# Kernel tuning notes

Measured on AMD Instinct MI355X. Metric: run time of the kernel, lower is better.

Reference implementation:

```python
import jax, jax.numpy as jnp
import numpy as np

E, H = 256, 4
DH = E // H                      # head dim 64
DHALF, N, R, K = 256, 16, 16, 5  # mamba d_inner//2, d_state, dt_rank, d_conv
B, L = 2, 2048


def _ln(x, g, b):
    m = jnp.mean(x, -1, keepdims=True)
    v = jnp.var(x, -1, keepdims=True)
    return (x - m) * jax.lax.rsqrt(v + 1e-5) * g + b


def _rotate_half(x):
    y = x.reshape(x.shape[:-1] + (-1, 2))
    return jnp.stack((-y[..., 1], y[..., 0]), -1).reshape(x.shape)


def _dwconv(x, w):  # x: (B,C,L), w: (C,1,K), depthwise 'same' conv, no bias (conv_bias//2 == 0)
    return jax.lax.conv_general_dilated(
        x, w, (1,), 'SAME', feature_group_count=x.shape[1],
        dimension_numbers=('NCH', 'OIH', 'NCH'))


def _selective_scan(x, dt, A_log, Bm, Cm, Dp, dt_bias):
    # x, dt: (B,Dh,L); Bm, Cm: (B,N,L); A_log: (Dh,N); Dp, dt_bias: (Dh,)
    A = -jnp.exp(A_log)
    delta = jax.nn.softplus(dt + dt_bias[None, :, None])
    seq = (jnp.moveaxis(delta, 2, 0), jnp.moveaxis(x, 2, 0),
           jnp.moveaxis(Bm, 2, 0), jnp.moveaxis(Cm, 2, 0))
    h0 = jnp.zeros((x.shape[0], A.shape[0], A.shape[1]), x.dtype)

    def step(h, inp):
        d_l, x_l, B_l, C_l = inp
        h = jnp.exp(d_l[:, :, None] * A) * h + (d_l * x_l)[:, :, None] * B_l[:, None, :]
        return h, jnp.einsum('bdn,bn->bd', h, C_l)

    _, ys = jax.lax.scan(step, h0, seq)
    return jnp.moveaxis(ys, 0, 2) + Dp[None, :, None] * x


def _forward(desc0, desc1, pe0, pe1, qkv_w, qkv_b, attn_out_w, attn_out_b,
             ma_ffn_w1, ma_ffn_b1, ma_ffn_g, ma_ffn_beta, ma_ffn_w2, ma_ffn_b2,
             m_in_w, m_convx_w, m_convz_w, m_xproj_w, m_dt_w, m_dt_b, m_Alog, m_D, m_out_w,
             ca_qk_w, ca_qk_b, ca_v_w, ca_v_b, ca_out_w, ca_out_b,
             ca_ffn_w1, ca_ffn_b1, ca_ffn_g, ca_ffn_beta, ca_ffn_w2, ca_ffn_b2):

    def mamba_twopath(x_in):
        xz = jnp.swapaxes(x_in @ m_in_w.T, 1, 2)           # (B, 2*Dh, L)
        xc, zc = xz[:, :DHALF], xz[:, DHALF:]
        xc = jax.nn.silu(_dwconv(xc, m_convx_w))
        zc = jax.nn.silu(_dwconv(zc, m_convz_w))
        x_dbl = jnp.einsum('bdl,kd->bkl', xc, m_xproj_w)   # (B, R+2N, L)
        # dt_proj applies its bias here AND the same bias is re-added inside the scan
        # (delta_bias), exactly as in the torch source.
        dt = jnp.einsum('brl,dr->bdl', x_dbl[:, :R], m_dt_w) + m_dt_b[None, :, None]
        Bm, Cm = x_dbl[:, R:R + N], x_dbl[:, R + N:]
        y = _selective_scan(xc, dt, m_Alog, Bm, Cm, m_D, m_dt_b)  # (B, Dh, L)
        return jnp.swapaxes(y, 1, 2) @ m_out_w.T, jnp.swapaxes(zc, 1, 2) @ m_out_w.T

    def ma_ffn(h):
        h = _ln(h @ ma_ffn_w1.T + ma_ffn_b1, ma_ffn_g, ma_ffn_beta)
        return jax.nn.gelu(h, approximate=False) @ ma_ffn_w2.T + ma_ffn_b2

    def mamba_attention(x, pe):
        b, l, _ = x.shape
        qkv = (x @ qkv_w.T + qkv_b).reshape(b, l, H, DH, 3)
        qkv = jnp.swapaxes(qkv, 1, 2)                       # (B,H,L,DH,3)
        q, k, v = qkv[..., 0], qkv[..., 1], qkv[..., 2]
        q = q * pe[0] + _rotate_half(q) * pe[1]
        k = k * pe[0] + _rotate_half(k) * pe[1]
        attn = jax.nn.softmax(jnp.einsum('bhid,bhjd->bhij', q, k) * DH ** -0.5, -1)
        o = jnp.einsum('bhij,bhjd->bhid', attn, v)
        o = jnp.swapaxes(o, 1, 2).reshape(b, l, E) @ attn_out_w.T + attn_out_b
        s_x, c_x = mamba_twopath(x)
        return x + ma_ffn(jnp.concatenate([x, o, s_x, c_x], -1))

    def ca_ffn(h):
        h = _ln(h @ ca_ffn_w1.T + ca_ffn_b1, ca_ffn_g, ca_ffn_beta)
        return jax.nn.gelu(h, approximate=False) @ ca_ffn_w2.T + ca_ffn_b2

    def split_heads(t):
        b, l, _ = t.shape
        return jnp.swapaxes(t.reshape(b, l, H, DH), 1, 2)

    def cross_attn(x0, x1):
        s = DH ** -0.25  # scale**0.5 applied to both qk0 and qk1
        qk0 = split_heads(x0 @ ca_qk_w.T + ca_qk_b) * s
        qk1 = split_heads(x1 @ ca_qk_w.T + ca_qk_b) * s
        v0 = split_heads(x0 @ ca_v_w.T + ca_v_b)
        v1 = split_heads(x1 @ ca_v_w.T + ca_v_b)
        sim = jnp.einsum('bhid,bhjd->bhij', qk0, qk1)       # (B,H,L0,L1)
        m0 = jnp.einsum('bhij,bhjd->bhid', jax.nn.softmax(sim, -1), v1)
        m1 = jnp.einsum('bhji,bhjd->bhid', jax.nn.softmax(sim, -2), v0)
        b, l = x0.shape[0], x0.shape[1]
        m0 = jnp.swapaxes(m0, 1, 2).reshape(b, l, E) @ ca_out_w.T + ca_out_b
        m1 = jnp.swapaxes(m1, 1, 2).reshape(b, x1.shape[1], E) @ ca_out_w.T + ca_out_b
        x0 = x0 + ca_ffn(jnp.concatenate([x0, m0], -1))
        x1 = x1 + ca_ffn(jnp.concatenate([x1, m1], -1))
        return x0, x1

    d0 = mamba_attention(desc0, pe0)
    d1 = mamba_attention(desc1, pe1)
    return cross_attn(d0, d1)


def setup_inputs():
    key = jax.random.key(0)
    ks = jax.random.split(key, 32)
    rn = lambda i, shape, s=0.02: jax.random.normal(ks[i], shape, jnp.float32) * s
    rng = np.random.default_rng(0)
    dt = np.exp(rng.uniform(size=DHALF) * (np.log(0.1) - np.log(0.001)) + np.log(0.001))
    inv_dt = dt + np.log(-np.expm1(-dt))
    return {
        'desc0': jax.random.normal(ks[0], (B, L, E), jnp.float32),
        'desc1': jax.random.normal(ks[1], (B, L, E), jnp.float32),
        'pe0': jax.random.normal(ks[2], (2, B, 1, L, DH), jnp.float32),
        'pe1': jax.random.normal(ks[3], (2, B, 1, L, DH), jnp.float32),
        'qkv_w': rn(4, (3 * E, E)), 'qkv_b': rn(5, (3 * E,)),
        'attn_out_w': rn(6, (E, E)), 'attn_out_b': rn(7, (E,)),
        'ma_ffn_w1': rn(8, (2 * E, 4 * E)), 'ma_ffn_b1': rn(9, (2 * E,)),
        'ma_ffn_g': jnp.ones((2 * E,), jnp.float32), 'ma_ffn_beta': jnp.zeros((2 * E,), jnp.float32),
        'ma_ffn_w2': rn(10, (E, 2 * E)), 'ma_ffn_b2': rn(11, (E,)),
        'm_in_w': rn(12, (2 * DHALF, E)),
        'm_convx_w': rn(13, (DHALF, 1, K), 0.2), 'm_convz_w': rn(14, (DHALF, 1, K), 0.2),
        'm_xproj_w': rn(15, (R + 2 * N, DHALF)),
        'm_dt_w': rn(16, (DHALF, R), R ** -0.5),
        'm_dt_b': jnp.asarray(inv_dt, jnp.float32),
        'm_Alog': jnp.log(jnp.broadcast_to(jnp.arange(1, N + 1, dtype=jnp.float32), (DHALF, N))),
        'm_D': jnp.ones((DHALF,), jnp.float32),
        'm_out_w': rn(17, (E, DHALF)),
        'ca_qk_w': rn(18, (E, E)), 'ca_qk_b': rn(19, (E,)),
        'ca_v_w': rn(20, (E, E)), 'ca_v_b': rn(21, (E,)),
        'ca_out_w': rn(22, (E, E)), 'ca_out_b': rn(23, (E,)),
        'ca_ffn_w1': rn(24, (2 * E, 2 * E)), 'ca_ffn_b1': rn(25, (2 * E,)),
        'ca_ffn_g': jnp.ones((2 * E,), jnp.float32), 'ca_ffn_beta': jnp.zeros((2 * E,), jnp.float32),
        'ca_ffn_w2': rn(26, (E, 2 * E)), 'ca_ffn_b2': rn(27, (E,)),
    }


def reference(desc0, desc1, pe0, pe1, qkv_w, qkv_b, attn_out_w, attn_out_b,
              ma_ffn_w1, ma_ffn_b1, ma_ffn_g, ma_ffn_beta, ma_ffn_w2, ma_ffn_b2,
              m_in_w, m_convx_w, m_convz_w, m_xproj_w, m_dt_w, m_dt_b, m_Alog, m_D, m_out_w,
              ca_qk_w, ca_qk_b, ca_v_w, ca_v_b, ca_out_w, ca_out_b,
              ca_ffn_w1, ca_ffn_b1, ca_ffn_g, ca_ffn_beta, ca_ffn_w2, ca_ffn_b2):
    return _forward(desc0, desc1, pe0, pe1, qkv_w, qkv_b, attn_out_w, attn_out_b,
                    ma_ffn_w1, ma_ffn_b1, ma_ffn_g, ma_ffn_beta, ma_ffn_w2, ma_ffn_b2,
                    m_in_w, m_convx_w, m_convz_w, m_xproj_w, m_dt_w, m_dt_b, m_Alog, m_D, m_out_w,
                    ca_qk_w, ca_qk_b, ca_v_w, ca_v_b, ca_out_w, ca_out_b,
                    ca_ffn_w1, ca_ffn_b1, ca_ffn_g, ca_ffn_beta, ca_ffn_w2, ca_ffn_b2)
```

## Files before the change

kernel.cpp:

```cpp
#include <hip/hip_runtime.h>

typedef unsigned short u16;
typedef short s16;
typedef s16 s16x8 __attribute__((ext_vector_type(8)));
typedef float f32x4 __attribute__((ext_vector_type(4)));

__device__ __forceinline__ float bf2f(u16 u){
  union { unsigned int i; float f; } v; v.i = ((unsigned int)u) << 16; return v.f;
}
__device__ __forceinline__ u16 f2bf(float f){
  union { float f; unsigned int u; } v; v.f = f;
  unsigned int r = (v.u + 0x7fffu + ((v.u >> 16) & 1u)) >> 16;
  return (u16)r;
}
__device__ __forceinline__ unsigned int cvtpk(float lo, float hi){
  unsigned int d;
  asm("v_cvt_pk_bf16_f32 %0, %1, %2" : "=v"(d) : "v"(lo), "v"(hi));
  return d;
}
__device__ __forceinline__ uint4 pack8(float4 a0, float4 a1){
  uint4 v;
  v.x = cvtpk(a0.x, a0.y); v.y = cvtpk(a0.z, a0.w);
  v.z = cvtpk(a1.x, a1.y); v.w = cvtpk(a1.z, a1.w);
  return v;
}
__device__ __forceinline__ float gelu_f(float x){
  return 0.5f * x * (1.f + erff(x * 0.70710678118654752440f));
}
__device__ __forceinline__ float ldw(const void* p, long i, int fl){
  return fl ? bf2f(((const u16*)p)[i]) : ((const float*)p)[i];
}
__device__ __forceinline__ float4 ldw4(const void* p, long i, int fl){
  if (fl){
    ushort4 w = *(const ushort4*)((const u16*)p + i);
    return make_float4(bf2f(w.x), bf2f(w.y), bf2f(w.z), bf2f(w.w));
  }
  return *(const float4*)((const float*)p + i);
}

template<int C>
__device__ __forceinline__ float dppf(float x){
  return __int_as_float(__builtin_amdgcn_update_dpp(0, __float_as_int(x), C, 0xf, 0xf, true));
}
__device__ __forceinline__ float dppmax16(float v){
  v = fmaxf(v, dppf<0xB1>(v));
  v = fmaxf(v, dppf<0x4E>(v));
  v = fmaxf(v, dppf<0x141>(v));
  v = fmaxf(v, dppf<0x140>(v));
  return v;
}
__device__ __forceinline__ float dppsum16(float v){
  v += dppf<0xB1>(v);
  v += dppf<0x4E>(v);
  v += dppf<0x141>(v);
  v += dppf<0x140>(v);
  return v;
}

__global__ __launch_bounds__(256) void k_sniff(const unsigned int* __restrict__ w,
                                               int n, int* __restrict__ flag){
  __shared__ int cnt[256];
  int c = 0;
  for (int i = threadIdx.x; i < n; i += 256){
    unsigned e = (w[i] >> 7) & 0xFFu;
    c += (e >= 120u && e <= 127u) ? 1 : 0;
  }
  cnt[threadIdx.x] = c; __syncthreads();
  for (int s = 128; s > 0; s >>= 1){
    if (threadIdx.x < s) cnt[threadIdx.x] += cnt[threadIdx.x + s];
    __syncthreads();
  }
  if (threadIdx.x == 0) flag[0] = (2 * cnt[0] > n) ? 1 : 0;
  if (threadIdx.x == 1) flag[1] = 0;
}

__global__ __launch_bounds__(256) void k_pad(
  const void* __restrict__ wx, const void* __restrict__ wd,
  const void* __restrict__ bd,
  float* __restrict__ px, float* __restrict__ pd, float* __restrict__ pb,
  const int* __restrict__ flagp)
{
  int fl = *flagp;
  int i = blockIdx.x * 256 + threadIdx.x;
  if (i < 16384){
    int r = i >> 8, c = i & 255;
    px[i] = (r < 48) ? ldw(wx, r*256 + c, fl) : 0.f;
  } else if (i < 32768){
    int j = i - 16384;
    int n = j >> 6, k = j & 63;
    pd[j] = (k < 16) ? ldw(wd, n*16 + k, fl) : 0.f;
  } else if (i < 33024){
    pb[i - 32768] = ldw(bd, i - 32768, fl);
  }
}

__global__ __launch_bounds__(256) void k_gemm_mfma(
  const void* __restrict__ A, int aflidx, int lda, int K, int N,
  const void* __restrict__ W, const void* __restrict__ W2, int nsplit, int wflidx,
  const void* __restrict__ bias,
  float* __restrict__ Cf, u16* __restrict__ Cb, int ldc,
  float* __restrict__ C2, int ldc2,
  const void* __restrict__ resid, int rflidx, int ldr,
  const void* __restrict__ csrc, int cflidx, float* __restrict__ cdst,
  float oscale, int act_gelu, int outmode, const int* __restrict__ flagp)
{
  const int fl  = flagp[0];
  const int afl = flagp[aflidx];
  const int wfl = flagp[wflidx];
  const int rfl = flagp[rflidx];
  const int cfl = flagp[cflidx];
  __shared__ u16 As[64*72];
  __shared__ u16 Bs[64*72];
  const int tid = threadIdx.x;
  const int w = tid >> 6, lane = tid & 63, quad = lane >> 4, m = lane & 15;
  const int m0 = blockIdx.y << 6, n0 = blockIdx.x << 6;
  const int srow = tid >> 2, sc0 = (tid & 3) << 4;
  const int reg2 = (n0 >= nsplit);
  const void* Wp = reg2 ? W2 : W;
  const int nbase = reg2 ? nsplit : 0;

  f32x4 acc[4];
  #pragma unroll
  for (int ct = 0; ct < 4; ++ct) acc[ct] = (f32x4){0.f,0.f,0.f,0.f};

  for (int k0 = 0; k0 < K; k0 += 64){
    {
      long ab = (long)(m0 + srow) * lda + k0 + sc0;
      if (afl && !act_gelu){
        #pragma unroll
        for (int g = 0; g < 2; ++g)
          *(uint4*)&As[srow*72 + sc0 + g*8] = *(const uint4*)((const u16*)A + ab + g*8);
      } else {
        #pragma unroll
        for (int g = 0; g < 2; ++g){
          float4 a0 = ldw4(A, ab + g*8, afl);
          float4 a1 = ldw4(A, ab + g*8 + 4, afl);
          if (act_gelu){
            a0.x=gelu_f(a0.x); a0.y=gelu_f(a0.y); a0.z=gelu_f(a0.z); a0.w=gelu_f(a0.w);
            a1.x=gelu_f(a1.x); a1.y=gelu_f(a1.y); a1.z=gelu_f(a1.z); a1.w=gelu_f(a1.w);
          }
          *(uint4*)&As[srow*72 + sc0 + g*8] = pack8(a0, a1);
        }
      }
    }
    {
      long wb = (long)(n0 + srow - nbase) * K + k0 + sc0;
      if (wfl){
        #pragma unroll
        for (int g = 0; g < 2; ++g)
          *(uint4*)&Bs[srow*72 + sc0 + g*8] = *(const uint4*)((const u16*)Wp + wb + g*8);
      } else {
        #pragma unroll
        for (int g = 0; g < 2; ++g){
          float4 b0 = *(const float4*)((const float*)Wp + wb + g*8);
          float4 b1 = *(const float4*)((const float*)Wp + wb + g*8 + 4);
          *(uint4*)&Bs[srow*72 + sc0 + g*8] = pack8(b0, b1);
        }
      }
    }
    __syncthreads();

    s16x8 av[2];
    #pragma unroll
    for (int s = 0; s < 2; ++s)
      av[s] = *(const s16x8*)&As[(w*16 + m)*72 + s*32 + quad*8];
    #pragma unroll
    for (int ct = 0; ct < 4; ++ct)
      #pragma unroll
      for (int s = 0; s < 2; ++s){
        s16x8 bv = *(const s16x8*)&Bs[(ct*16 + m)*72 + s*32 + quad*8];
        acc[ct] = __builtin_amdgcn_mfma_f32_16x16x32_bf16(av[s], bv, acc[ct], 0, 0, 0);
      }
    __syncthreads();
  }

  #pragma unroll
  for (int r = 0; r < 4; ++r){
    int gm = m0 + w*16 + quad*4 + r;
    #pragma unroll
    for (int ct = 0; ct < 4; ++ct){
      int gn = n0 + ct*16 + m;
      float v = acc[ct][r];
      if (reg2){
        C2[(long)gm * ldc2 + (gn - nsplit)] = v;
      } else if (outmode == 4){
        float bv = ldw(bias, gn, wfl);
        float dl = v + bv + bv;
        float delta = (dl > 20.f) ? dl : __logf(1.f + __expf(dl));
        Cf[(long)gm * ldc + gn] = delta;
        C2[(long)gm * ldc2 + gn] = delta * ldw(resid, (long)gm * ldr + gn, rfl);
      } else {
        if (bias) v += ldw(bias, gn, wfl);
        v *= oscale;
        if (resid) v += ldw(resid, (long)gm * ldr + gn, rfl);
        long off = (long)gm * ldc + gn;
        if (outmode == 2){
          if (fl) Cb[off] = f2bf(v); else Cf[off] = v;
        } else if (outmode == 3){
          Cb[off] = f2bf(v);
        } else {
          Cf[off] = v;
        }
        if (cdst) cdst[(long)gm * ldc + gn] = ldw(csrc, (long)gm * 256 + gn, cfl);
      }
    }
  }
}

struct GB8 {
  const float* A[8]; const void* W[8]; const void* bias[8];
  float* Cf[8]; u16* Cb[8]; const void* resid[8];
  const void* csrc[8]; float* cdst[8]; float osc[8];
  int cfl[8]; int wkoff[8]; int rfli[8];
};

__global__ __launch_bounds__(256) void k_gemmb(
  GB8 gb, int lda, int K, int N, int ldc, int ldr, int ldwq,
  int act_gelu, int outmode, const int* __restrict__ flagp)
{
  const int fl = flagp[0];
  const int z = blockIdx.z;
  const float* A = gb.A[z]; const void* W = gb.W[z]; const void* bias = gb.bias[z];
  float* Cf = gb.Cf[z]; u16* Cb = gb.Cb[z]; const void* resid = gb.resid[z];
  const void* csrc = gb.csrc[z]; float* cdst = gb.cdst[z];
  const float osc = gb.osc[z];
  const int cfl = flagp[gb.cfl[z]];
  const int rfl = flagp[gb.rfli[z]];
  const int wkoff = gb.wkoff[z];

  __shared__ u16 As[64*72];
  __shared__ u16 Bs[64*72];
  const int tid = threadIdx.x;
  const int w = tid >> 6, lane = tid & 63, quad = lane >> 4, m = lane & 15;
  const int m0 = blockIdx.y << 6, n0 = blockIdx.x << 6;
  const int srow = tid >> 2, sc0 = (tid & 3) << 4;

  f32x4 acc[4];
  #pragma unroll
  for (int ct = 0; ct < 4; ++ct) acc[ct] = (f32x4){0.f,0.f,0.f,0.f};

  for (int k0 = 0; k0 < K; k0 += 64){
    {
      const float* ar = A + (long)(m0 + srow) * lda + k0 + sc0;
      #pragma unroll
      for (int g = 0; g < 2; ++g){
        float4 a0 = *(const float4*)(ar + g*8);
        float4 a1 = *(const float4*)(ar + g*8 + 4);
        if (act_gelu){
          a0.x=gelu_f(a0.x); a0.y=gelu_f(a0.y); a0.z=gelu_f(a0.z); a0.w=gelu_f(a0.w);
          a1.x=gelu_f(a1.x); a1.y=gelu_f(a1.y); a1.z=gelu_f(a1.z); a1.w=gelu_f(a1.w);
        }
        *(uint4*)&As[srow*72 + sc0 + g*8] = pack8(a0, a1);
      }
    }
    {
      long wb = (long)(n0 + srow) * ldwq + wkoff + k0 + sc0;
      if (fl){
        #pragma unroll
        for (int g = 0; g < 2; ++g)
          *(uint4*)&Bs[srow*72 + sc0 + g*8] = *(const uint4*)((const u16*)W + wb + g*8);
      } else {
        #pragma unroll
        for (int g = 0; g < 2; ++g){
          float4 b0 = *(const float4*)((const float*)W + wb + g*8);
          float4 b1 = *(const float4*)((const float*)W + wb + g*8 + 4);
          *(uint4*)&Bs[srow*72 + sc0 + g*8] = pack8(b0, b1);
        }
      }
    }
    __syncthreads();

    s16x8 av[2];
    #pragma unroll
    for (int s = 0; s < 2; ++s)
      av[s] = *(const s16x8*)&As[(w*16 + m)*72 + s*32 + quad*8];
    #pragma unroll
    for (int ct = 0; ct < 4; ++ct)
      #pragma unroll
      for (int s = 0; s < 2; ++s){
        s16x8 bv = *(const s16x8*)&Bs[(ct*16 + m)*72 + s*32 + quad*8];
        acc[ct] = __builtin_amdgcn_mfma_f32_16x16x32_bf16(av[s], bv, acc[ct], 0, 0, 0);
      }
    __syncthreads();
  }

  #pragma unroll
  for (int r = 0; r < 4; ++r){
    int gm = m0 + w*16 + quad*4 + r;
    #pragma unroll
    for (int ct = 0; ct < 4; ++ct){
      int gn = n0 + ct*16 + m;
      float v = acc[ct][r];
      if (bias) v += ldw(bias, gn, fl);
      v *= osc;
      if (resid) v += ldw(resid, (long)gm * ldr + gn, rfl);
      long off = (long)gm * ldc + gn;
      if (outmode == 2){
        if (fl) Cb[off] = f2bf(v); else Cf[off] = v;
      } else if (outmode == 3){
        Cb[off] = f2bf(v);
      } else {
        Cf[off] = v;
      }
      if (cdst) cdst[(long)gm * ldc + gn] = ldw(csrc, (long)gm * 256 + gn, cfl);
    }
  }
}

__global__ __launch_bounds__(256) void k_rope(
  const float* __restrict__ qkv0, const float* __restrict__ qkv1,
  const void* __restrict__ pe0, const void* __restrict__ pe1,
  u16* __restrict__ q, u16* __restrict__ k, u16* __restrict__ v,
  int L, int B, int H, const int* __restrict__ flagp)
{
  int fl = *flagp;
  int tid = threadIdx.x;
  int lq = tid >> 6, d = tid & 63;
  int l = blockIdx.x * 4 + lq;
  int bh = blockIdx.y;
  int dsc = bh >> 3;
  int bh7 = bh & 7;
  int b = bh7 >> 2, h = bh7 & 3;
  const float* qkv = dsc ? qkv1 : qkv0;
  const void* pe = dsc ? pe1 : pe0;
  const float* row = qkv + ((long)b * L + l) * 768 + h * 192;
  float qv = row[d*3+0], kv = row[d*3+1], vv = row[d*3+2];
  int dn = (d & 1) ? (d - 1) : (d + 1);
  float qn = row[dn*3+0], kn = row[dn*3+1];
  float rq = (d & 1) ? qn : -qn;
  float rk = (d & 1) ? kn : -kn;
  long peo = ((long)b * L + l) * 64 + d;
  float p0 = ldw(pe, peo, fl);
  float p1 = ldw(pe, (long)B * L * 64 + peo, fl);
  long o = ((long)bh * L + l) * 64 + d;
  q[o] = f2bf((qv * p0 + rq * p1) * 0.125f);
  k[o] = f2bf(kv * p0 + rk * p1);
  v[o] = f2bf(vv);
}

__global__ __launch_bounds__(256, 8) void k_attn_mfma(
  const u16* __restrict__ Q, long qsb, long qsh, long qsl,
  const u16* __restrict__ Kp, long ksb, long ksh, long ksl,
  const u16* __restrict__ Vp, long vsb, long vsh, long vsl,
  float* __restrict__ Opart, float* __restrict__ mpart, float* __restrict__ lpart,
  int L, int H, int kchunk)
{
  __shared__ u16 Kt[64*72];
  __shared__ u16 Vt[64*72];
  __shared__ u16 Ps[64*72];
  const int tid  = threadIdx.x;
  const int w    = tid >> 6;
  const int lane = tid & 63;
  const int quad = lane >> 4;
  const int m    = lane & 15;
  const int bh = blockIdx.y, b = bh / H, h = bh % H;
  const int iq0 = blockIdx.x * 64;
  const int z = blockIdx.z;
  const long BHL = (long)gridDim.y * L;

  const u16* Qb = Q  + b*qsb + h*qsh;
  const u16* Kb = Kp + b*ksb + h*ksh;
  const u16* Vb = Vp + b*vsb + h*vsh;

  s16x8 aq[2];
  {
    const u16* qr = Qb + (long)(iq0 + w*16 + m) * qsl + quad*8;
    aq[0] = *(const s16x8*)(qr);
    aq[1] = *(const s16x8*)(qr + 32);
  }

  f32x4 o_acc[4];
  #pragma unroll
  for (int nt = 0; nt < 4; ++nt) o_acc[nt] = (f32x4){0.f,0.f,0.f,0.f};
  float mrow[4] = {-1e30f,-1e30f,-1e30f,-1e30f};
  float lrow[4] = {0.f,0.f,0.f,0.f};

  const int srow = tid >> 2, sc0 = (tid & 3) << 4;
  const int kg = tid & 15;
  const int dg = tid >> 4;
  const int vcb = ((((dg >> 2) * 2) + (kg >> 1)) & 7) * 8 + (kg & 1) * 4;
  const int modd = m & 1;
  const int pcolb = m & 6;
  const int jend = z * kchunk + kchunk;

  for (int j0 = z * kchunk; j0 < jend; j0 += 64){
    {
      const u16* kr = Kb + (long)(j0 + srow) * ksl + sc0;
      *(uint4*)&Kt[srow*72 + sc0]     = *(const uint4*)kr;
      *(uint4*)&Kt[srow*72 + sc0 + 8] = *(const uint4*)(kr + 8);
      const u16* vr = Vb + (long)(j0 + 4*kg) * vsl + 4*dg;
      ushort4 r0 = *(const ushort4*)(vr);
      ushort4 r1 = *(const ushort4*)(vr + vsl);
      ushort4 r2 = *(const ushort4*)(vr + 2*vsl);
      ushort4 r3 = *(const ushort4*)(vr + 3*vsl);
      u16* vt = &Vt[(4*dg)*72 + vcb];
      *(ushort4*)(vt)       = make_ushort4(r0.x, r1.x, r2.x, r3.x);
      *(ushort4*)(vt + 72)  = make_ushort4(r0.y, r1.y, r2.y, r3.y);
      *(ushort4*)(vt + 144) = make_ushort4(r0.z, r1.z, r2.z, r3.z);
      *(ushort4*)(vt + 216) = make_ushort4(r0.w, r1.w, r2.w, r3.w);
    }
    __syncthreads();

    float sv[4][4];
    #pragma unroll
    for (int ct = 0; ct < 4; ++ct){
      f32x4 acc = (f32x4){0.f,0.f,0.f,0.f};
      #pragma unroll
      for (int s = 0; s < 2; ++s){
        s16x8 bk = *(const s16x8*)&Kt[(ct*16 + m)*72 + s*32 + quad*8];
        acc = __builtin_amdgcn_mfma_f32_16x16x32_bf16(aq[s], bk, acc, 0, 0, 0);
      }
      #pragma unroll
      for (int r = 0; r < 4; ++r) sv[ct][r] = acc[r];
    }

    float v0s[4];
    int need = 0;
    #pragma unroll
    for (int r = 0; r < 4; ++r){
      float v0 = fmaxf(fmaxf(sv[0][r], sv[1][r]), fmaxf(sv[2][r], sv[3][r]));
      v0 = dppmax16(v0);
      v0s[r] = v0;
      need |= (v0 > mrow[r] + 8.f) ? 1 : 0;
    }
    if (__any(need)){
      float alpha[4];
      #pragma unroll
      for (int r = 0; r < 4; ++r){
        float mn = fmaxf(mrow[r], v0s[r]);
        alpha[r] = __expf(mrow[r] - mn);
        mrow[r] = mn;
        lrow[r] *= alpha[r];
      }
      #pragma unroll
      for (int nt = 0; nt < 4; ++nt)
        #pragma unroll
        for (int r = 0; r < 4; ++r) o_acc[nt][r] *= alpha[r];
    }
    float rsum[4] = {0.f,0.f,0.f,0.f};
    #pragma unroll
    for (int ct = 0; ct < 4; ++ct)
      #pragma unroll
      for (int r = 0; r < 4; ++r){
        float p = __expf(sv[ct][r] - mrow[r]);
        sv[ct][r] = p;
        rsum[r] += p;
      }
    #pragma unroll
    for (int r = 0; r < 4; ++r)
      lrow[r] += dppsum16(rsum[r]);

    #pragma unroll
    for (int ct = 0; ct < 4; ++ct){
      const int kb = (2*w + 2*ct + (m >> 3)) & 7;
      const int col = (kb << 3) | pcolb;
      #pragma unroll
      for (int rr = 0; rr < 2; ++rr){
        float nb_lo = dppf<0xB1>(sv[ct][rr]);
        float nb_hi = dppf<0xB1>(sv[ct][2+rr]);
        float lo = modd ? nb_hi       : sv[ct][rr];
        float hi = modd ? sv[ct][2+rr] : nb_lo;
        unsigned int pk = cvtpk(lo, hi);
        int row = w*16 + quad*4 + rr + 2*modd;
        *(unsigned int*)&Ps[row*72 + col] = pk;
      }
    }
    asm volatile("s_waitcnt lgkmcnt(0)" ::: "memory");

    s16x8 ap[2];
    #pragma unroll
    for (int s = 0; s < 2; ++s)
      ap[s] = *(const s16x8*)&Ps[(w*16 + m)*72 + (((2*w + 4*s + quad) & 7) << 3)];
    #pragma unroll
    for (int nt = 0; nt < 4; ++nt)
      #pragma unroll
      for (int s = 0; s < 2; ++s){
        s16x8 bv = *(const s16x8*)&Vt[(nt*16 + m)*72 + (((2*nt + 4*s + quad) & 7) << 3)];
        o_acc[nt] = __builtin_amdgcn_mfma_f32_16x16x32_bf16(ap[s], bv, o_acc[nt], 0, 0, 0);
      }
    __syncthreads();
  }

  const long zOoff = (long)z * BHL * 64;
  #pragma unroll
  for (int r = 0; r < 4; ++r){
    int iq = iq0 + w*16 + quad*4 + r;
    long rowid = ((long)b*L + iq) * H + h;
    #pragma unroll
    for (int nt = 0; nt < 4; ++nt)
      Opart[zOoff + rowid*64 + nt*16 + m] = o_acc[nt][r];
    if (m == 0){
      mpart[(long)z*BHL + rowid] = mrow[r];
      lpart[(long)z*BHL + rowid] = lrow[r];
    }
  }
}

__global__ __launch_bounds__(256) void k_attn_comb(
  const float* Opart, const float* mpart, const float* lpart,
  float* O, long BHL)
{
  long i = (long)blockIdx.x * 256 + threadIdx.x;
  long row = i >> 6;
  float mv[4];
  float M = -1e30f;
  #pragma unroll
  for (int z = 0; z < 4; ++z){
    mv[z] = mpart[(long)z*BHL + row];
    M = fmaxf(M, mv[z]);
  }
  long N64 = BHL * 64;
  float T = 0.f, acc = 0.f;
  #pragma unroll
  for (int z = 0; z < 4; ++z){
    float wz = __expf(mv[z] - M);
    T   += lpart[(long)z*BHL + row] * wz;
    acc += Opart[(long)z*N64 + i] * wz;
  }
  O[i] = acc / T;
}

__global__ __launch_bounds__(256) void k_conv2(
  const float* __restrict__ xz,
  const void* __restrict__ wx, const void* __restrict__ wz,
  float* __restrict__ outx, float* __restrict__ outz,
  int L, const int* __restrict__ flagp)
{
  int fl = *flagp;
  int c = threadIdx.x;
  int bl = blockIdx.x; int b = bl / L, l = bl % L;
  int choff = blockIdx.y ? 256 : 0;
  const void* w = blockIdx.y ? wz : wx;
  float* out = blockIdx.y ? outz : outx;
  const float* base = xz + ((long)b * L) * 512 + choff + c;
  float s = 0.f;
  #pragma unroll
  for (int kk = 0; kk < 5; ++kk){
    int ll = l + kk - 2;
    if (ll >= 0 && ll < L) s += base[(long)ll * 512] * ldw(w, c*5 + kk, fl);
  }
  out[((long)b * L + l) * 256 + c] = s / (1.f + __expf(-s));
}

#define SC_CS 64
#define SC_NC 32

__global__ __launch_bounds__(256) void k_scan1(
  const float* __restrict__ delta, const float* __restrict__ dxc,
  const float* __restrict__ xdbl, const void* __restrict__ Alog,
  float* __restrict__ E_out, float* __restrict__ F_out,
  int L, const int* __restrict__ flagp)
{
  int fl = *flagp;
  int tid = threadIdx.x;
  int g = tid >> 4, n = tid & 15;
  int gid = blockIdx.x * 16 + g;
  int chunk = gid & (SC_NC - 1);
  int p = gid >> 5;
  int b = p >> 8, d = p & 255;
  float A = -__expf(ldw(Alog, d*16 + n, fl));
  const float* dtp = delta + (long)b*L*256 + d;
  const float* dxp = dxc   + (long)b*L*256 + d;
  const float* xdb = xdbl + (long)b*L*64;
  int l0 = chunk * SC_CS;
  float E = 1.f, F = 0.f;
  for (int i = 0; i < SC_CS; i += 4){
    float e[4], u[4];
    #pragma unroll
    for (int j = 0; j < 4; ++j){
      int l = l0 + i + j;
      e[j] = __expf(dtp[(long)l*256] * A);
      u[j] = dxp[(long)l*256] * xdb[l*64 + 16 + n];
    }
    F = e[0]*F + u[0]; F = e[1]*F + u[1];
    F = e[2]*F + u[2]; F = e[3]*F + u[3];
    E *= (e[0]*e[1]) * (e[2]*e[3]);
  }
  long idx = (long)(p*16 + n) * SC_NC + chunk;
  E_out[idx] = E; F_out[idx] = F;
}

__global__ __launch_bounds__(256) void k_scan2(
  const float* __restrict__ E, const float* __restrict__ F,
  float* __restrict__ Hin)
{
  int pn = blockIdx.x * 256 + threadIdx.x;
  const float* Ep = E + (long)pn * SC_NC;
  const float* Fp = F + (long)pn * SC_NC;
  float* Hp = Hin + (long)pn * SC_NC;
  float h = 0.f;
  #pragma unroll
  for (int c = 0; c < SC_NC; ++c){
    Hp[c] = h;
    h = Ep[c] * h + Fp[c];
  }
}

__global__ __launch_bounds__(256) void k_scan3(
  const float* __restrict__ delta, const float* __restrict__ dxc,
  const float* __restrict__ xc, const float* __restrict__ xdbl,
  const void* __restrict__ Alog, const void* __restrict__ Dp,
  const float* __restrict__ Hin, float* __restrict__ y,
  int L, const int* __restrict__ flagp)
{
  int fl = *flagp;
  int tid = threadIdx.x;
  int g = tid >> 4, n = tid & 15;
  int gid = blockIdx.x * 16 + g;
  int chunk = gid & (SC_NC - 1);
  int p = gid >> 5;
  int b = p >> 8, d = p & 255;
  float A = -__expf(ldw(Alog, d*16 + n, fl));
  float Dv = ldw(Dp, d, fl);
  const float* dtp = delta + (long)b*L*256 + d;
  const float* dxp = dxc   + (long)b*L*256 + d;
  const float* xcb = xc    + (long)b*L*256 + d;
  const float* xdb = xdbl + (long)b*L*64;
  float* yb = y + (long)b*L*256 + d;
  long idx = (long)(p*16 + n) * SC_NC + chunk;
  float h = Hin[idx];
  int l0 = chunk * SC_CS;
  for (int i = 0; i < SC_CS; i += 4){
    float e[4], u[4], cm[4], xv[4];
    #pragma unroll
    for (int j = 0; j < 4; ++j){
      int l = l0 + i + j;
      e[j]  = __expf(dtp[(long)l*256] * A);
      u[j]  = dxp[(long)l*256] * xdb[l*64 + 16 + n];
      cm[j] = xdb[l*64 + 32 + n];
      xv[j] = xcb[(long)l*256];
    }
    float s0, s1, s2, s3;
    h = e[0]*h + u[0]; s0 = h * cm[0];
    h = e[1]*h + u[1]; s1 = h * cm[1];
    h = e[2]*h + u[2]; s2 = h * cm[2];
    h = e[3]*h + u[3]; s3 = h * cm[3];
    s0 += __shfl_xor(s0, 1, 16); s1 += __shfl_xor(s1, 1, 16);
    s2 += __shfl_xor(s2, 1, 16); s3 += __shfl_xor(s3, 1, 16);
    s0 += __shfl_xor(s0, 2, 16); s1 += __shfl_xor(s1, 2, 16);
    s2 += __shfl_xor(s2, 2, 16); s3 += __shfl_xor(s3, 2, 16);
    s0 += __shfl_xor(s0, 4, 16); s1 += __shfl_xor(s1, 4, 16);
    s2 += __shfl_xor(s2, 4, 16); s3 += __shfl_xor(s3, 4, 16);
    s0 += __shfl_xor(s0, 8, 16); s1 += __shfl_xor(s1, 8, 16);
    s2 += __shfl_xor(s2, 8, 16); s3 += __shfl_xor(s3, 8, 16);
    if (n < 4){
      float out = (n == 0) ? s0 + Dv*xv[0] : (n == 1) ? s1 + Dv*xv[1]
                : (n == 2) ? s2 + Dv*xv[2] : s3 + Dv*xv[3];
      yb[(long)(l0 + i + n)*256] = out;
    }
  }
}

__global__ __launch_bounds__(256) void k_ln2(
  float* __restrict__ hA, const float* __restrict__ hA2,
  float* __restrict__ hB, const float* __restrict__ hB2,
  const void* __restrict__ g, const void* __restrict__ beta,
  const int* __restrict__ flagp)
{
  int fl = *flagp;
  int r = blockIdx.x * 4 + (threadIdx.x >> 6);
  float* hbase = (r < 4096) ? hA : hB;
  const float* h2base = (r < 4096) ? hA2 : hB2;
  int row = r & 4095;
  int lane = threadIdx.x & 63;
  float* hr = hbase + (long)row * 512;
  const float* h2r = h2base + (long)row * 512;
  float v[8]; float s = 0.f, ss = 0.f;
  #pragma unroll
  for (int i = 0; i < 8; ++i){
    v[i] = hr[lane + 64*i] + h2r[lane + 64*i];
    s += v[i]; ss += v[i]*v[i];
  }
  #pragma unroll
  for (int off = 1; off < 64; off <<= 1){ s += __shfl_xor(s, off); ss += __shfl_xor(ss, off); }
  float mean = s * (1.f/512.f);
  float var  = ss * (1.f/512.f) - mean * mean;
  float rs = rsqrtf(var + 1e-5f);
  #pragma unroll
  for (int i = 0; i < 8; ++i){
    int c = lane + 64*i;
    hr[c] = (v[i] - mean) * rs * ldw(g, c, fl) + ldw(beta, c, fl);
  }
}

extern "C" void kernel_launch(void* const* d_in, const int* in_sizes, int n_in,
                              void* d_out, int out_size, void* d_ws, size_t ws_size,
                              hipStream_t stream)
{
  const int B_ = 2, L_ = 2048, H_ = 4;
  const long BLE = (long)B_ * L_ * 256;
  const long BHLb = 2L * B_ * H_ * L_;
  const long BHLc = (long)B_ * H_ * L_;

  int* flagp = (int*)d_ws;
  float* base = (float*)d_ws + 64;

  float* cat0   = base + 0*BLE;
  float* cat1   = base + 3*BLE;
  float* xz01   = base + 6*BLE;
  u16*   q01    = (u16*)(base + 10*BLE);
  u16*   k01    = (u16*)(base + 11*BLE);
  u16*   v01    = (u16*)(base + 12*BLE);
  float* Opart  = base + 13*BLE;
  float* ob01   = base + 21*BLE;
  float* mml    = base + 23*BLE;
  float* mll    = mml + 4*32768;
  float* xc01   = base + 24*BLE;
  float* zc01   = base + 26*BLE;
  float* xdbl01 = base + 28*BLE;
  float* delta01= base + 29*BLE;
  float* dxc01  = base + 31*BLE;
  float* scE    = base + 33*BLE;
  float* scF    = scE + 524288;
  float* scH    = scF + 524288;
  float* y01    = base + 35*BLE;
  float* catc0  = base + 37*BLE;
  float* catc1  = base + 41*BLE;
  float* h0     = base + 45*BLE;
  float* part0  = base + 47*BLE;
  float* h1     = base + 49*BLE;
  float* part1  = base + 51*BLE;
  float* dbuf0  = base + 53*BLE;
  float* dbuf1  = base + 54*BLE;
  u16*   qc     = (u16*)(base + 55*BLE);
  u16*   kc     = qc + 1048576;
  u16*   vc     = kc + 1048576;
  u16*   oc     = vc + 1048576;
  float* catA   = base + 57*BLE;
  float* catB   = base + 59*BLE;
  float* px     = base + 61*BLE;
  float* pd     = px + 16384;
  float* pb     = pd + 16384;

  const void* in[35];
  for (int i = 0; i < 35 && i < n_in; ++i) in[i] = d_in[i];

  k_sniff<<<1, 256, 0, stream>>>((const unsigned int*)in[0], 2048, flagp);
  k_pad<<<130, 256, 0, stream>>>(in[17], in[18], in[19], px, pd, pb, flagp);

  const int BIG = 1 << 30;
  const long sbP = (long)H_ * L_ * 64, shP = (long)L_ * 64, slP = 64;
  const long sbF = (long)L_ * 256,     shF = 64,            slF = 256;
  const int kchunk = L_ / 4;

  k_gemm_mfma<<<dim3(20, 64), 256, 0, stream>>>(
      in[0], 0, 256, 256, 1280, in[4], in[14], 768, 0, in[5],
      cat0, nullptr, 768, xz01, 512,
      nullptr, 1, 0, nullptr, 1, nullptr, 1.f, 0, 0, flagp);
  k_gemm_mfma<<<dim3(20, 64), 256, 0, stream>>>(
      in[1], 0, 256, 256, 1280, in[4], in[14], 768, 0, in[5],
      cat1, nullptr, 768, xz01 + 2*BLE, 512,
      nullptr, 1, 0, nullptr, 1, nullptr, 1.f, 0, 0, flagp);
  k_rope<<<dim3(L_/4, 16), 256, 0, stream>>>(cat0, cat1, in[2], in[3],
      q01, k01, v01, L_, B_, H_, flagp);
  k_attn_mfma<<<dim3(L_/64, 16, 4), 256, 0, stream>>>(
      q01, sbP, shP, slP, k01, sbP, shP, slP, v01, sbP, shP, slP,
      Opart, mml, mll, L_, H_, kchunk);
  k_attn_comb<<<8192, 256, 0, stream>>>(Opart, mml, mll, ob01, BHLb);
  k_conv2<<<dim3(2*B_*L_, 2), 256, 0, stream>>>(xz01, in[15], in[16], xc01, zc01, L_, flagp);
  k_gemm_mfma<<<dim3(1, 128), 256, 0, stream>>>(
      xc01, 1, 256, 256, 64, px, nullptr, BIG, 1, nullptr,
      xdbl01, nullptr, 64, nullptr, 0,
      nullptr, 1, 0, nullptr, 1, nullptr, 1.f, 0, 0, flagp);
  k_gemm_mfma<<<dim3(4, 128), 256, 0, stream>>>(
      xdbl01, 1, 64, 64, 256, pd, nullptr, BIG, 1, pb,
      delta01, nullptr, 256, dxc01, 256,
      xc01, 1, 256, nullptr, 1, nullptr, 1.f, 0, 4, flagp);
  k_scan1<<<2048, 256, 0, stream>>>(delta01, dxc01, xdbl01, in[20], scE, scF, L_, flagp);
  k_scan2<<<64, 256, 0, stream>>>(scE, scF, scH);
  k_scan3<<<2048, 256, 0, stream>>>(delta01, dxc01, xc01, xdbl01, in[20], in[21], scH, y01, L_, flagp);
  {
    GB8 gb = {};
    gb.A[0] = y01;        gb.W[0] = in[22]; gb.Cf[0] = catc0 + 512; gb.osc[0] = 1.f; gb.cfl[0] = 1;
    gb.A[1] = zc01;       gb.W[1] = in[22]; gb.Cf[1] = catc0 + 768; gb.osc[1] = 1.f; gb.cfl[1] = 1;
    gb.A[2] = ob01;       gb.W[2] = in[6];  gb.bias[2] = in[7];     gb.Cf[2] = catc0 + 256;
    gb.csrc[2] = in[0];   gb.cdst[2] = catc0; gb.osc[2] = 1.f;      gb.cfl[2] = 0;
    gb.A[3] = y01 + BLE;  gb.W[3] = in[22]; gb.Cf[3] = catc1 + 512; gb.osc[3] = 1.f; gb.cfl[3] = 1;
    gb.A[4] = zc01 + BLE; gb.W[4] = in[22]; gb.Cf[4] = catc1 + 768; gb.osc[4] = 1.f; gb.cfl[4] = 1;
    gb.A[5] = ob01 + BLE; gb.W[5] = in[6];  gb.bias[5] = in[7];     gb.Cf[5] = catc1 + 256;
    gb.csrc[5] = in[1];   gb.cdst[5] = catc1; gb.osc[5] = 1.f;      gb.cfl[5] = 0;
    k_gemmb<<<dim3(4, 64, 6), 256, 0, stream>>>(gb, 256, 256, 256, 1024, 0, 256, 0, 0, flagp);
  }
  {
    GB8 gb = {};
    gb.cfl[0] = gb.cfl[1] = gb.cfl[2] = gb.cfl[3] = 1;
    gb.A[0] = catc0;       gb.W[0] = in[8]; gb.bias[0] = in[9]; gb.Cf[0] = h0;    gb.osc[0] = 1.f;
    gb.A[1] = catc0 + 512; gb.W[1] = in[8]; gb.wkoff[1] = 512;  gb.Cf[1] = part0; gb.osc[1] = 1.f;
    gb.A[2] = catc1;       gb.W[2] = in[8]; gb.bias[2] = in[9]; gb.Cf[2] = h1;    gb.osc[2] = 1.f;
    gb.A[3] = catc1 + 512; gb.W[3] = in[8]; gb.wkoff[3] = 512;  gb.Cf[3] = part1; gb.osc[3] = 1.f;
    k_gemmb<<<dim3(8, 64, 4), 256, 0, stream>>>(gb, 1024, 512, 512, 512, 0, 1024, 0, 0, flagp);
  }
  k_ln2<<<2048, 256, 0, stream>>>(h0, part0, h1, part1, in[10], in[11], flagp);
  {
    GB8 gb = {};
    gb.cfl[0] = gb.cfl[1] = 1;
    gb.A[0] = h0; gb.W[0] = in[12]; gb.bias[0] = in[13]; gb.resid[0] = in[0]; gb.rfli[0] = 0;
    gb.Cf[0] = dbuf0; gb.osc[0] = 1.f;
    gb.A[1] = h1; gb.W[1] = in[12]; gb.bias[1] = in[13]; gb.resid[1] = in[1]; gb.rfli[1] = 0;
    gb.Cf[1] = dbuf1; gb.osc[1] = 1.f;
    k_gemmb<<<dim3(4, 64, 2), 256, 0, stream>>>(gb, 512, 512, 256, 256, 256, 512, 1, 0, flagp);
  }

  const float s4 = 0.35355339059327373f;
  float* cm0 = xc01;
  float* cm1 = xc01 + BLE;
  {
    GB8 gb = {};
    gb.cfl[0] = gb.cfl[1] = gb.cfl[2] = gb.cfl[3] = 1;
    gb.A[0] = dbuf0; gb.W[0] = in[23]; gb.bias[0] = in[24]; gb.Cb[0] = qc; gb.osc[0] = s4;
    gb.A[1] = dbuf1; gb.W[1] = in[23]; gb.bias[1] = in[24]; gb.Cb[1] = kc; gb.osc[1] = s4;
    gb.A[2] = dbuf0; gb.W[2] = in[25]; gb.bias[2] = in[26]; gb.Cb[2] = vc; gb.osc[2] = 1.f;
    gb.A[3] = dbuf1; gb.W[3] = in[25]; gb.bias[3] = in[26]; gb.Cb[3] = oc; gb.osc[3] = 1.f;
    k_gemmb<<<dim3(4, 64, 4), 256, 0, stream>>>(gb, 256, 256, 256, 256, 0, 256, 0, 3, flagp);
  }
  k_attn_mfma<<<dim3(L_/64, B_*H_, 4), 256, 0, stream>>>(
      qc, sbF, shF, slF, kc, sbF, shF, slF, oc, sbF, shF, slF,
      Opart, mml, mll, L_, H_, kchunk);
  k_attn_comb<<<4096, 256, 0, stream>>>(Opart, mml, mll, cm0, BHLc);
  k_attn_mfma<<<dim3(L_/64, B_*H_, 4), 256, 0, stream>>>(
      kc, sbF, shF, slF, qc, sbF, shF, slF, vc, sbF, shF, slF,
      Opart, mml, mll, L_, H_, kchunk);
  k_attn_comb<<<4096, 256, 0, stream>>>(Opart, mml, mll, cm1, BHLc);
  {
    GB8 gb = {};
    gb.cfl[0] = gb.cfl[1] = 1;
    gb.A[0] = cm0; gb.W[0] = in[27]; gb.bias[0] = in[28]; gb.Cf[0] = catA + 256;
    gb.csrc[0] = dbuf0; gb.cdst[0] = catA; gb.osc[0] = 1.f;
    gb.A[1] = cm1; gb.W[1] = in[27]; gb.bias[1] = in[28]; gb.Cf[1] = catB + 256;
    gb.csrc[1] = dbuf1; gb.cdst[1] = catB; gb.osc[1] = 1.f;
    k_gemmb<<<dim3(4, 64, 2), 256, 0, stream>>>(gb, 256, 256, 256, 512, 0, 256, 0, 0, flagp);
  }
  {
    GB8 gb = {};
    gb.cfl[0] = gb.cfl[1] = gb.cfl[2] = gb.cfl[3] = 1;
    gb.A[0] = catA;       gb.W[0] = in[29]; gb.bias[0] = in[30]; gb.Cf[0] = h0;    gb.osc[0] = 1.f;
    gb.A[1] = catA + 256; gb.W[1] = in[29]; gb.wkoff[1] = 256;   gb.Cf[1] = part0; gb.osc[1] = 1.f;
    gb.A[2] = catB;       gb.W[2] = in[29]; gb.bias[2] = in[30]; gb.Cf[2] = h1;    gb.osc[2] = 1.f;
    gb.A[3] = catB + 256; gb.W[3] = in[29]; gb.wkoff[3] = 256;   gb.Cf[3] = part1; gb.osc[3] = 1.f;
    k_gemmb<<<dim3(8, 64, 4), 256, 0, stream>>>(gb, 512, 256, 512, 512, 0, 512, 0, 0, flagp);
  }
  k_ln2<<<2048, 256, 0, stream>>>(h0, part0, h1, part1, in[31], in[32], flagp);
  {
    GB8 gb = {};
    gb.cfl[0] = gb.cfl[1] = 1;
    gb.rfli[0] = gb.rfli[1] = 1;
    gb.A[0] = h0; gb.W[0] = in[33]; gb.bias[0] = in[34]; gb.resid[0] = dbuf0;
    gb.Cf[0] = (float*)d_out; gb.Cb[0] = (u16*)d_out; gb.osc[0] = 1.f;
    gb.A[1] = h1; gb.W[1] = in[33]; gb.bias[1] = in[34]; gb.resid[1] = dbuf1;
    gb.Cf[1] = (float*)d_out + BLE; gb.Cb[1] = (u16*)d_out + BLE; gb.osc[1] = 1.f;
    k_gemmb<<<dim3(4, 64, 2), 256, 0, stream>>>(gb, 512, 512, 256, 256, 256, 512, 1, 2, flagp);
  }
}
```

Baseline: 706.0 us.

## Store delta and dx transposed for contiguous scan reads; fold D*x into out-proj

The delta/dt GEMM epilogue now writes delta and delta*x in a channel-major (d, b*L) layout, so the scan kernels read four consecutive timesteps with one float4 load instead of strided 256-apart loads. The D*x skip term moves out of the scan and into the out-projection GEMM's A-tile loading through a new aux pointer and D vector. This cuts strided global traffic in both scan passes. In exchange the epilogue stores become column-strided, and the batched GEMM does extra loads on those slices.

```diff
diff --git a/kernel.cpp b/kernel.cpp
--- a/kernel.cpp
+++ b/kernel.cpp
@@ -174,6 +174,26 @@
     __syncthreads();
   }
 
+  if (outmode == 4){
+    const int gmb = m0 + w*16 + quad*4;
+    #pragma unroll
+    for (int ct = 0; ct < 4; ++ct){
+      int gn = n0 + ct*16 + m;
+      float bv = ldw(bias, gn, wfl);
+      float dl4[4], dx4[4];
+      #pragma unroll
+      for (int r = 0; r < 4; ++r){
+        float dl = acc[ct][r] + bv + bv;
+        float delta = (dl > 20.f) ? dl : __logf(1.f + __expf(dl));
+        dl4[r] = delta;
+        dx4[r] = delta * ldw(resid, (long)(gmb + r) * ldr + gn, rfl);
+      }
+      *(float4*)&Cf[(long)gn * ldc + gmb] = make_float4(dl4[0], dl4[1], dl4[2], dl4[3]);
+      *(float4*)&C2[(long)gn * ldc2 + gmb] = make_float4(dx4[0], dx4[1], dx4[2], dx4[3]);
+    }
+    return;
+  }
+
   #pragma unroll
   for (int r = 0; r < 4; ++r){
     int gm = m0 + w*16 + quad*4 + r;
@@ -183,12 +203,6 @@
       float v = acc[ct][r];
       if (reg2){
         C2[(long)gm * ldc2 + (gn - nsplit)] = v;
-      } else if (outmode == 4){
-        float bv = ldw(bias, gn, wfl);
-        float dl = v + bv + bv;
-        float delta = (dl > 20.f) ? dl : __logf(1.f + __expf(dl));
-        Cf[(long)gm * ldc + gn] = delta;
-        C2[(long)gm * ldc2 + gn] = delta * ldw(resid, (long)gm * ldr + gn, rfl);
       } else {
         if (bias) v += ldw(bias, gn, wfl);
         v *= oscale;
@@ -212,6 +226,7 @@
   float* Cf[8]; u16* Cb[8]; const void* resid[8];
   const void* csrc[8]; float* cdst[8]; float osc[8];
   int cfl[8]; int wkoff[8]; int rfli[8];
+  const float* aux[8]; const void* dvec;
 };
 
 __global__ __launch_bounds__(256) void k_gemmb(
@@ -227,6 +242,7 @@
   const int cfl = flagp[gb.cfl[z]];
   const int rfl = flagp[gb.rfli[z]];
   const int wkoff = gb.wkoff[z];
+  const float* aux = gb.aux[z];
 
   __shared__ u16 As[64*72];
   __shared__ u16 Bs[64*72];
@@ -246,6 +262,15 @@
       for (int g = 0; g < 2; ++g){
         float4 a0 = *(const float4*)(ar + g*8);
         float4 a1 = *(const float4*)(ar + g*8 + 4);
+        if (aux){
+          const float* xr = aux + (long)(m0 + srow) * lda + k0 + sc0;
+          float4 x0 = *(const float4*)(xr + g*8);
+          float4 x1 = *(const float4*)(xr + g*8 + 4);
+          float4 d0 = ldw4(gb.dvec, k0 + sc0 + g*8, fl);
+          float4 d1 = ldw4(gb.dvec, k0 + sc0 + g*8 + 4, fl);
+          a0.x += d0.x*x0.x; a0.y += d0.y*x0.y; a0.z += d0.z*x0.z; a0.w += d0.w*x0.w;
+          a1.x += d1.x*x1.x; a1.y += d1.y*x1.y; a1.z += d1.z*x1.z; a1.w += d1.w*x1.w;
+        }
         if (act_gelu){
           a0.x=gelu_f(a0.x); a0.y=gelu_f(a0.y); a0.z=gelu_f(a0.z); a0.w=gelu_f(a0.w);
           a1.x=gelu_f(a1.x); a1.y=gelu_f(a1.y); a1.z=gelu_f(a1.z); a1.w=gelu_f(a1.w);
@@ -546,10 +571,10 @@
 #define SC_NC 32
 
 __global__ __launch_bounds__(256) void k_scan1(
-  const float* __restrict__ delta, const float* __restrict__ dxc,
+  const float* __restrict__ deltaT, const float* __restrict__ dxcT,
   const float* __restrict__ xdbl, const void* __restrict__ Alog,
   float* __restrict__ E_out, float* __restrict__ F_out,
-  int L, const int* __restrict__ flagp)
+  int L, int ldt, const int* __restrict__ flagp)
 {
   int fl = *flagp;
   int tid = threadIdx.x;
@@ -559,19 +584,22 @@
   int p = gid >> 5;
   int b = p >> 8, d = p & 255;
   float A = -__expf(ldw(Alog, d*16 + n, fl));
-  const float* dtp = delta + (long)b*L*256 + d;
-  const float* dxp = dxc   + (long)b*L*256 + d;
+  const float* dTp = deltaT + (long)d*ldt + (long)b*L;
+  const float* dxp = dxcT  + (long)d*ldt + (long)b*L;
   const float* xdb = xdbl + (long)b*L*64;
   int l0 = chunk * SC_CS;
   float E = 1.f, F = 0.f;
   for (int i = 0; i < SC_CS; i += 4){
+    int l = l0 + i;
+    float4 dt4 = *(const float4*)(dTp + l);
+    float4 dx4 = *(const float4*)(dxp + l);
     float e[4], u[4];
-    #pragma unroll
-    for (int j = 0; j < 4; ++j){
-      int l = l0 + i + j;
-      e[j] = __expf(dtp[(long)l*256] * A);
-      u[j] = dxp[(long)l*256] * xdb[l*64 + 16 + n];
-    }
+    e[0] = __expf(dt4.x * A); e[1] = __expf(dt4.y * A);
+    e[2] = __expf(dt4.z * A); e[3] = __expf(dt4.w * A);
+    u[0] = dx4.x * xdb[(l+0)*64 + 16 + n];
+    u[1] = dx4.y * xdb[(l+1)*64 + 16 + n];
+    u[2] = dx4.z * xdb[(l+2)*64 + 16 + n];
+    u[3] = dx4.w * xdb[(l+3)*64 + 16 + n];
     F = e[0]*F + u[0]; F = e[1]*F + u[1];
     F = e[2]*F + u[2]; F = e[3]*F + u[3];
     E *= (e[0]*e[1]) * (e[2]*e[3]);
@@ -597,11 +625,10 @@
 }
 
 __global__ __launch_bounds__(256) void k_scan3(
-  const float* __restrict__ delta, const float* __restrict__ dxc,
-  const float* __restrict__ xc, const float* __restrict__ xdbl,
-  const void* __restrict__ Alog, const void* __restrict__ Dp,
+  const float* __restrict__ deltaT, const float* __restrict__ dxcT,
+  const float* __restrict__ xdbl, const void* __restrict__ Alog,
   const float* __restrict__ Hin, float* __restrict__ y,
-  int L, const int* __restrict__ flagp)
+  int L, int ldt, const int* __restrict__ flagp)
 {
   int fl = *flagp;
   int tid = threadIdx.x;
@@ -611,25 +638,28 @@
   int p = gid >> 5;
   int b = p >> 8, d = p & 255;
   float A = -__expf(ldw(Alog, d*16 + n, fl));
-  float Dv = ldw(Dp, d, fl);
-  const float* dtp = delta + (long)b*L*256 + d;
-  const float* dxp = dxc   + (long)b*L*256 + d;
-  const float* xcb = xc    + (long)b*L*256 + d;
+  const float* dTp = deltaT + (long)d*ldt + (long)b*L;
+  const float* dxp = dxcT  + (long)d*ldt + (long)b*L;
   const float* xdb = xdbl + (long)b*L*64;
   float* yb = y + (long)b*L*256 + d;
   long idx = (long)(p*16 + n) * SC_NC + chunk;
   float h = Hin[idx];
   int l0 = chunk * SC_CS;
   for (int i = 0; i < SC_CS; i += 4){
-    float e[4], u[4], cm[4], xv[4];
-    #pragma unroll
-    for (int j = 0; j < 4; ++j){
-      int l = l0 + i + j;
-      e[j]  = __expf(dtp[(long)l*256] * A);
-      u[j]  = dxp[(long)l*256] * xdb[l*64 + 16 + n];
-      cm[j] = xdb[l*64 + 32 + n];
-      xv[j] = xcb[(long)l*256];
-    }
+    int l = l0 + i;
+    float4 dt4 = *(const float4*)(dTp + l);
+    float4 dx4 = *(const float4*)(dxp + l);
+    float e[4], u[4], cm[4];
+    e[0] = __expf(dt4.x * A); e[1] = __expf(dt4.y * A);
+    e[2] = __expf(dt4.z * A); e[3] = __expf(dt4.w * A);
+    u[0] = dx4.x * xdb[(l+0)*64 + 16 + n];
+    u[1] = dx4.y * xdb[(l+1)*64 + 16 + n];
+    u[2] = dx4.z * xdb[(l+2)*64 + 16 + n];
+    u[3] = dx4.w * xdb[(l+3)*64 + 16 + n];
+    cm[0] = xdb[(l+0)*64 + 32 + n];
+    cm[1] = xdb[(l+1)*64 + 32 + n];
+    cm[2] = xdb[(l+2)*64 + 32 + n];
+    cm[3] = xdb[(l+3)*64 + 32 + n];
     float s0, s1, s2, s3;
     h = e[0]*h + u[0]; s0 = h * cm[0];
     h = e[1]*h + u[1]; s1 = h * cm[1];
@@ -644,9 +674,8 @@
     s0 += __shfl_xor(s0, 8, 16); s1 += __shfl_xor(s1, 8, 16);
     s2 += __shfl_xor(s2, 8, 16); s3 += __shfl_xor(s3, 8, 16);
     if (n < 4){
-      float out = (n == 0) ? s0 + Dv*xv[0] : (n == 1) ? s1 + Dv*xv[1]
-                : (n == 2) ? s2 + Dv*xv[2] : s3 + Dv*xv[3];
-      yb[(long)(l0 + i + n)*256] = out;
+      float out = (n == 0) ? s0 : (n == 1) ? s1 : (n == 2) ? s2 : s3;
+      yb[(long)(l + n)*256] = out;
     }
   }
 }
@@ -742,6 +771,7 @@
   const long sbP = (long)H_ * L_ * 64, shP = (long)L_ * 64, slP = 64;
   const long sbF = (long)L_ * 256,     shF = 64,            slF = 256;
   const int kchunk = L_ / 4;
+  const int MROWS = 4 * L_;
 
   k_gemm_mfma<<<dim3(20, 64), 256, 0, stream>>>(
       in[0], 0, 256, 256, 1280, in[4], in[14], 768, 0, in[5],
@@ -764,18 +794,19 @@
       nullptr, 1, 0, nullptr, 1, nullptr, 1.f, 0, 0, flagp);
   k_gemm_mfma<<<dim3(4, 128), 256, 0, stream>>>(
       xdbl01, 1, 64, 64, 256, pd, nullptr, BIG, 1, pb,
-      delta01, nullptr, 256, dxc01, 256,
+      delta01, nullptr, MROWS, dxc01, MROWS,
       xc01, 1, 256, nullptr, 1, nullptr, 1.f, 0, 4, flagp);
-  k_scan1<<<2048, 256, 0, stream>>>(delta01, dxc01, xdbl01, in[20], scE, scF, L_, flagp);
+  k_scan1<<<2048, 256, 0, stream>>>(delta01, dxc01, xdbl01, in[20], scE, scF, L_, MROWS, flagp);
   k_scan2<<<64, 256, 0, stream>>>(scE, scF, scH);
-  k_scan3<<<2048, 256, 0, stream>>>(delta01, dxc01, xc01, xdbl01, in[20], in[21], scH, y01, L_, flagp);
+  k_scan3<<<2048, 256, 0, stream>>>(delta01, dxc01, xdbl01, in[20], scH, y01, L_, MROWS, flagp);
   {
     GB8 gb = {};
-    gb.A[0] = y01;        gb.W[0] = in[22]; gb.Cf[0] = catc0 + 512; gb.osc[0] = 1.f; gb.cfl[0] = 1;
+    gb.dvec = in[21];
+    gb.A[0] = y01;        gb.aux[0] = xc01;       gb.W[0] = in[22]; gb.Cf[0] = catc0 + 512; gb.osc[0] = 1.f; gb.cfl[0] = 1;
     gb.A[1] = zc01;       gb.W[1] = in[22]; gb.Cf[1] = catc0 + 768; gb.osc[1] = 1.f; gb.cfl[1] = 1;
     gb.A[2] = ob01;       gb.W[2] = in[6];  gb.bias[2] = in[7];     gb.Cf[2] = catc0 + 256;
     gb.csrc[2] = in[0];   gb.cdst[2] = catc0; gb.osc[2] = 1.f;      gb.cfl[2] = 0;
-    gb.A[3] = y01 + BLE;  gb.W[3] = in[22]; gb.Cf[3] = catc1 + 512; gb.osc[3] = 1.f; gb.cfl[3] = 1;
+    gb.A[3] = y01 + BLE;  gb.aux[3] = xc01 + BLE; gb.W[3] = in[22]; gb.Cf[3] = catc1 + 512; gb.osc[3] = 1.f; gb.cfl[3] = 1;
     gb.A[4] = zc01 + BLE; gb.W[4] = in[22]; gb.Cf[4] = catc1 + 768; gb.osc[4] = 1.f; gb.cfl[4] = 1;
     gb.A[5] = ob01 + BLE; gb.W[5] = in[6];  gb.bias[5] = in[7];     gb.Cf[5] = catc1 + 256;
     gb.csrc[5] = in[1];   gb.cdst[5] = catc1; gb.osc[5] = 1.f;      gb.cfl[5] = 0;
```

New measurement: 657.8 us. 6.8% less time.
